# Optimization experiments

Hardware: AMD Instinct MI355X
Metric: run time of the kernel (lower is better)

## Reference

```python
import jax, jax.numpy as jnp
import numpy as np
from jax import lax

SCALE_R = 1.0
LOCAL_MAX_THR = 0.1
BORDER = 5
MAX_NUM_CENTERS = 2048  # 16 * 128
DILATIONS = (1, 4, 16)
NEG_INF = -1e9


def _conv2d(x, w, d):
    # x: [B,1,H,W], w: [1,1,3,3], dilation d, SAME padding
    return lax.conv_general_dilated(
        x, w, window_strides=(1, 1), padding='SAME', rhs_dilation=(d, d),
        dimension_numbers=('NCHW', 'OIHW', 'NCHW'))


def _avg3(x):
    s = lax.reduce_window(x, 0.0, lax.add, (1, 1, 3, 3), (1, 1, 1, 1), 'SAME')
    return s * (1.0 / 9.0)


def _maxpool3(x):
    return lax.reduce_window(x, -jnp.inf, lax.max, (1, 1, 3, 3), (1, 1, 1, 1), 'SAME')


def setup_inputs() -> dict:
    key = jax.random.key(0)
    k1, k2, k3 = jax.random.split(key, 3)
    inp = jax.random.normal(k1, (8, 3, 1024, 1024), dtype=jnp.float32)
    w_c = jax.random.normal(k2, (3, 1, 1, 3, 3), dtype=jnp.float32) * 0.1
    w_s = jax.random.normal(k3, (3, 1, 1, 3, 3), dtype=jnp.float32) * 0.1
    return {'input': inp, 'w_c': w_c, 'w_s': w_s}


def reference(input, w_c, w_s):
    B, _, H, W = input.shape
    S = input[:, 0:1]          # sin direction field
    C = input[:, 1:2]          # cos direction field
    # R = inverse_log_r(scale_r * R_raw) = exp(scale_r * r) - 1
    R = jnp.exp(SCALE_R * input[:, 2:3]) - 1.0
    output = jnp.concatenate([S, C, R], axis=1)  # input with R channel replaced

    # multiscale localization: learned 3x3 convs at several dilations over C and S
    resp = jnp.zeros_like(S)
    for i, d in enumerate(DILATIONS):
        resp = resp + _conv2d(C, w_c[i], d) + _conv2d(S, w_s[i], d)
    conv_resp = jax.nn.relu(resp)  # [B,1,H,W] center heatmap

    # local-max selection: smooth, compare against 3x3 max, threshold, exclude border
    smooth = _avg3(conv_resp)
    is_peak = (smooth >= _maxpool3(smooth)) & (smooth > LOCAL_MAX_THR)
    border = jnp.zeros((H, W), dtype=bool).at[BORDER:H - BORDER, BORDER:W - BORDER].set(True)
    is_peak = is_peak & border[None, None]

    # per-batch top-K centers by response score (vectorized NMS/top-k)
    flat = conv_resp.reshape(B, H * W)
    scores = jnp.where(is_peak.reshape(B, H * W), flat, NEG_INF)
    vals, idx = lax.top_k(scores, MAX_NUM_CENTERS)          # [B, K]
    valid = (vals > LOCAL_MAX_THR).astype(flat.dtype)
    x = (idx % W).astype(flat.dtype) * valid
    y = (idx // W).astype(flat.dtype) * valid
    v = vals * valid
    # packed centers: [valid_flag, x, y, score, score] -> [B, K, 5]
    center_pred = jnp.stack([valid, x, y, v, v], axis=-1)
    return output, center_pred, conv_resp
```

## Files before the change

kernel.cpp:

```cpp
#include <hip/hip_runtime.h>
#include <cstdint>

typedef unsigned int u32;
typedef unsigned long long u64;

#define BATCH 8
#define H 1024
#define W 1024
#define HW (H*W)
#define NPIX (BATCH*HW)
#define KTOP 2048
#define NBIN 8192
#define KEYCAP 8192
#define CAPP 131072
#define CAPC 65536
#define TARGET 2080

#define D9 1e-3f
#define DV 1e-4f

#define TOX 64
#define TOY 32
#define CCX 72
#define CCY 36
#define SCSTR 76
#define SIROWS 68
#define SICOLS 104
#define SISTR 104
#define NJT 3
#define CAPB 768

#define MP(b) ((b)*16)
#define MC(b) (128 + (b)*16)
#define MK(b) (256 + (b)*16)
#define MT(b) (384 + (b)*16)

#define OFF_MISC 0
#define OFF_PASS 4096
#define OFF_CHK  (OFF_PASS + (size_t)BATCH*CAPP*8)
#define OFF_KEY  (OFF_CHK  + (size_t)BATCH*CAPC*8)

#define LD4(p) (*reinterpret_cast<const float4*>(p))
#define ST4(p,v) (*reinterpret_cast<float4*>(p) = (v))

__device__ __forceinline__ double conv_resp_f64(
    const float* __restrict__ in, const float* __restrict__ wc,
    const float* __restrict__ wsw, int b, int y, int x)
{
  const float* base = in + (size_t)b * 3 * HW;
  const float* Sp = base;
  const float* Cp = base + HW;
  double resp = 0.0;
  const int dil[3] = {1, 4, 16};
  #pragma unroll
  for (int di = 0; di < 3; ++di) {
    int d = dil[di];
    double ac = 0.0, as = 0.0;
    #pragma unroll
    for (int ky = 0; ky < 3; ++ky) {
      int yy = y + (ky - 1) * d;
      bool yok = ((unsigned)yy < (unsigned)H);
      #pragma unroll
      for (int kx = 0; kx < 3; ++kx) {
        int xx = x + (kx - 1) * d;
        bool ok = yok && ((unsigned)xx < (unsigned)W);
        double a  = ok ? (double)Cp[yy * W + xx] : 0.0;
        double s2 = ok ? (double)Sp[yy * W + xx] : 0.0;
        ac = fma(a,  (double)wc[di * 9 + ky * 3 + kx], ac);
        as = fma(s2, (double)wsw[di * 9 + ky * 3 + kx], as);
      }
    }
    resp += ac;
    resp += as;
  }
  return resp > 0.0 ? resp : 0.0;
}

__device__ __forceinline__ u64 make_key(double val, int p) {
  u64 dbits = __double_as_longlong(val);
  return (dbits & ~0xFFFFFull) | (u64)((~(u32)p) & 0xFFFFFu);
}

__device__ __forceinline__ void stage_ch(
    float* sIn, const float* __restrict__ src, int tx0, int ty0, int tid)
{
  const int NG = (SIROWS * SICOLS) / 4;
  for (int g = tid; g < NG; g += 256) {
    int r = g / (SICOLS / 4);
    int c4 = (g - r * (SICOLS / 4)) * 4;
    int gy = ty0 - 18 + r;
    int gx0 = tx0 - 20 + c4;
    float4 v = make_float4(0.f, 0.f, 0.f, 0.f);
    if ((unsigned)gy < (unsigned)H) {
      if (gx0 >= 0 && gx0 + 3 < W) {
        v = LD4(src + gy * W + gx0);
      } else {
        float t[4];
        #pragma unroll
        for (int i = 0; i < 4; ++i) {
          int gx = gx0 + i;
          t[i] = ((unsigned)gx < (unsigned)W) ? src[gy * W + gx] : 0.f;
        }
        v = make_float4(t[0], t[1], t[2], t[3]);
      }
    }
    *reinterpret_cast<float4*>(&sIn[r * SISTR + c4]) = v;
  }
}

__device__ __forceinline__ void accum_taps4(
    const float* sIn, const float* __restrict__ wp, float part[NJT][4], int tid)
{
  #pragma unroll
  for (int k = 0; k < NJT; ++k) {
    int j = k * 256 + tid;
    if (j < (CCX / 4) * CCY) {
      int cr = j / (CCX / 4);
      int cc0 = (j - cr * (CCX / 4)) * 4;
      const float* base = sIn + (cr + 16) * SISTR + cc0 + 16;

      float4 a1L = LD4(base - SISTR - 4),      a1M = LD4(base - SISTR),      a1R = LD4(base - SISTR + 4);
      float4 b1L = LD4(base + SISTR - 4),      b1M = LD4(base + SISTR),      b1R = LD4(base + SISTR + 4);
      float4 a4L = LD4(base - 4 * SISTR - 4),  a4M = LD4(base - 4 * SISTR),  a4R = LD4(base - 4 * SISTR + 4);
      float4 b4L = LD4(base + 4 * SISTR - 4),  b4M = LD4(base + 4 * SISTR),  b4R = LD4(base + 4 * SISTR + 4);
      float4 gAa = LD4(base - 16 * SISTR - 16), gAm = LD4(base - 16 * SISTR), gAb = LD4(base - 16 * SISTR + 16);
      float4 gBa = LD4(base + 16 * SISTR - 16), gBm = LD4(base + 16 * SISTR), gBb = LD4(base + 16 * SISTR + 16);
      float4 zA = LD4(base - 16), zL = LD4(base - 4), zM = LD4(base), zR = LD4(base + 4), zB = LD4(base + 16);

      float wm1[12] = {a1L.x,a1L.y,a1L.z,a1L.w, a1M.x,a1M.y,a1M.z,a1M.w, a1R.x,a1R.y,a1R.z,a1R.w};
      float wp1[12] = {b1L.x,b1L.y,b1L.z,b1L.w, b1M.x,b1M.y,b1M.z,b1M.w, b1R.x,b1R.y,b1R.z,b1R.w};
      float wm4[12] = {a4L.x,a4L.y,a4L.z,a4L.w, a4M.x,a4M.y,a4M.z,a4M.w, a4R.x,a4R.y,a4R.z,a4R.w};
      float wp4[12] = {b4L.x,b4L.y,b4L.z,b4L.w, b4M.x,b4M.y,b4M.z,b4M.w, b4R.x,b4R.y,b4R.z,b4R.w};
      float wz [12] = {zL.x,zL.y,zL.z,zL.w, zM.x,zM.y,zM.z,zM.w, zR.x,zR.y,zR.z,zR.w};
      float vAa[4] = {gAa.x,gAa.y,gAa.z,gAa.w};
      float vAm[4] = {gAm.x,gAm.y,gAm.z,gAm.w};
      float vAb[4] = {gAb.x,gAb.y,gAb.z,gAb.w};
      float vBa[4] = {gBa.x,gBa.y,gBa.z,gBa.w};
      float vBm[4] = {gBm.x,gBm.y,gBm.z,gBm.w};
      float vBb[4] = {gBb.x,gBb.y,gBb.z,gBb.w};
      float vzA[4] = {zA.x,zA.y,zA.z,zA.w};
      float vzB[4] = {zB.x,zB.y,zB.z,zB.w};

      #pragma unroll
      for (int i = 0; i < 4; ++i) {
        float ac = 0.f;
        ac = fmaf(wm1[i + 3], wp[0], ac);
        ac = fmaf(wm1[i + 4], wp[1], ac);
        ac = fmaf(wm1[i + 5], wp[2], ac);
        ac = fmaf(wz [i + 3], wp[3], ac);
        ac = fmaf(wz [i + 4], wp[4], ac);
        ac = fmaf(wz [i + 5], wp[5], ac);
        ac = fmaf(wp1[i + 3], wp[6], ac);
        ac = fmaf(wp1[i + 4], wp[7], ac);
        ac = fmaf(wp1[i + 5], wp[8], ac);
        float a = ac;
        ac = 0.f;
        ac = fmaf(wm4[i + 0], wp[9],  ac);
        ac = fmaf(wm4[i + 4], wp[10], ac);
        ac = fmaf(wm4[i + 8], wp[11], ac);
        ac = fmaf(wz [i + 0], wp[12], ac);
        ac = fmaf(wz [i + 4], wp[13], ac);
        ac = fmaf(wz [i + 8], wp[14], ac);
        ac = fmaf(wp4[i + 0], wp[15], ac);
        ac = fmaf(wp4[i + 4], wp[16], ac);
        ac = fmaf(wp4[i + 8], wp[17], ac);
        a += ac;
        ac = 0.f;
        ac = fmaf(vAa[i], wp[18], ac);
        ac = fmaf(vAm[i], wp[19], ac);
        ac = fmaf(vAb[i], wp[20], ac);
        ac = fmaf(vzA[i], wp[21], ac);
        ac = fmaf(wz[i + 4], wp[22], ac);
        ac = fmaf(vzB[i], wp[23], ac);
        ac = fmaf(vBa[i], wp[24], ac);
        ac = fmaf(vBm[i], wp[25], ac);
        ac = fmaf(vBb[i], wp[26], ac);
        a += ac;
        part[k][i] += a;
      }
    }
  }
}

__global__ __launch_bounds__(256, 4) void conv_screen_kernel(
    const float* __restrict__ in, const float* __restrict__ wc,
    const float* __restrict__ wsw, float* __restrict__ out0,
    float* __restrict__ convr, u64* __restrict__ passlist,
    u64* __restrict__ checklist, u32* __restrict__ misc)
{
  __shared__ __align__(16) float uni[SIROWS * SISTR];

  float* sIn = uni;
  float (*sconv)[SCSTR] = (float (*)[SCSTR])uni;
  u64* pbuf = (u64*)(uni + 2752);
  u64* cbuf = (u64*)(uni + 2752 + 2 * CAPB);
  u32* lcnt = (u32*)(uni + 2752 + 4 * CAPB);

  int b = blockIdx.z;
  int tx0 = blockIdx.x * TOX;
  int ty0 = blockIdx.y * TOY;
  int tid = threadIdx.x;
  const float* Sp = in + (size_t)b * 3 * HW;
  const float* Cp = Sp + HW;
  const float* Rp = Sp + 2 * HW;
  float* ob = out0 + (size_t)b * 3 * HW;
  float* cb = convr + (size_t)b * HW;

  #pragma unroll
  for (int r = 0; r < (TOX * TOY) / 4 / 256; ++r) {
    int idx = r * 256 + tid;
    int ly = idx / (TOX / 4);
    int lx4 = (idx - ly * (TOX / 4)) * 4;
    int p0 = (ty0 + ly) * W + tx0 + lx4;
    float4 S4 = LD4(Sp + p0);
    float4 C4 = LD4(Cp + p0);
    float4 R4 = LD4(Rp + p0);
    ST4(ob + p0, S4);
    ST4(ob + HW + p0, C4);
    float4 E4 = make_float4(expf(R4.x) - 1.f, expf(R4.y) - 1.f,
                            expf(R4.z) - 1.f, expf(R4.w) - 1.f);
    ST4(ob + 2 * HW + p0, E4);
  }

  float part[NJT][4];
  #pragma unroll
  for (int k = 0; k < NJT; ++k)
    #pragma unroll
    for (int i = 0; i < 4; ++i) part[k][i] = 0.f;

  stage_ch(sIn, Cp, tx0, ty0, tid);
  __syncthreads();
  accum_taps4(sIn, wc, part, tid);
  __syncthreads();
  stage_ch(sIn, Sp, tx0, ty0, tid);
  __syncthreads();
  accum_taps4(sIn, wsw, part, tid);
  __syncthreads();

  if (tid < 4) lcnt[tid] = 0;
  #pragma unroll
  for (int k = 0; k < NJT; ++k) {
    int j = k * 256 + tid;
    if (j < (CCX / 4) * CCY) {
      int cr = j / (CCX / 4);
      int cc0 = (j - cr * (CCX / 4)) * 4;
      float4 rv = make_float4(fmaxf(part[k][0], 0.f), fmaxf(part[k][1], 0.f),
                              fmaxf(part[k][2], 0.f), fmaxf(part[k][3], 0.f));
      *reinterpret_cast<float4*>(&sconv[cr][cc0]) = rv;
      if (cr >= 2 && cr <= CCY - 3 && cc0 >= 4 && cc0 <= 64) {
        int gy = ty0 - 2 + cr, gx0 = tx0 - 4 + cc0;
        ST4(cb + gy * W + gx0, rv);
      }
    }
  }
  __syncthreads();

  for (int r = 0; r < (TOX * TOY) / 256; ++r) {
    int idx = r * 256 + tid;
    int ly = idx >> 6;
    int lx = idx & 63;
    int x = tx0 + lx, y = ty0 + ly;
    bool act = (y >= 5 && y <= H - 6 && x >= 5 && x <= W - 6);

    bool cand = false, pass = false;
    float val = 0.f;
    if (act) {
      float vs0[5], vs1[5], vs2[5];
      #pragma unroll
      for (int j = 0; j < 5; ++j) {
        int c = lx + 2 + j;
        float a0 = sconv[ly + 0][c];
        float a1 = sconv[ly + 1][c];
        float a2 = sconv[ly + 2][c];
        float a3 = sconv[ly + 3][c];
        float a4 = sconv[ly + 4][c];
        vs0[j] = a0 + a1 + a2;
        vs1[j] = a1 + a2 + a3;
        vs2[j] = a2 + a3 + a4;
      }
      float hs0[3], hs1[3], hs2[3];
      #pragma unroll
      for (int j = 0; j < 3; ++j) {
        hs0[j] = vs0[j] + vs0[j + 1] + vs0[j + 2];
        hs1[j] = vs1[j] + vs1[j + 1] + vs1[j + 2];
        hs2[j] = vs2[j] + vs2[j + 1] + vs2[j + 2];
      }
      float sc9 = hs1[1];
      val = sconv[ly + 2][lx + 4];
      float m9 = fmaxf(fmaxf(fmaxf(hs0[0], hs0[1]), fmaxf(hs0[2], hs1[0])),
                       fmaxf(fmaxf(hs1[2], hs2[0]), fmaxf(hs2[1], hs2[2])));
      cand = !((sc9 < 0.9f - D9) || (sc9 < m9 - D9) || (val < 0.1f - DV));
      pass = cand && (sc9 > 0.9f + D9) && (sc9 >= m9 + D9) && (val > 0.1f + DV);
    }

    u64 entry = ((u64)__float_as_uint(val) << 32) | (u32)(y * W + x);
    if (pass) {
      u32 pos = atomicAdd(&lcnt[0], 1u);
      if (pos < CAPB) pbuf[pos] = entry;
      else {
        u32 g = atomicAdd(&misc[MP(b)], 1u);
        if (g < CAPP) passlist[(size_t)b * CAPP + g] = entry;
      }
    } else if (cand) {
      u32 pos = atomicAdd(&lcnt[1], 1u);
      if (pos < CAPB) cbuf[pos] = entry;
      else {
        u32 g = atomicAdd(&misc[MC(b)], 1u);
        if (g < CAPC) checklist[(size_t)b * CAPC + g] = entry;
      }
    }
  }
  __syncthreads();

  u32 np = min(lcnt[0], (u32)CAPB);
  u32 nc = min(lcnt[1], (u32)CAPB);
  if (tid == 0) lcnt[2] = np ? atomicAdd(&misc[MP(b)], np) : 0u;
  if (tid == 1) lcnt[3] = nc ? atomicAdd(&misc[MC(b)], nc) : 0u;
  __syncthreads();
  u32 pbase = lcnt[2], cbase = lcnt[3];

  for (u32 i = tid; i < np; i += 256) {
    u32 g = pbase + i;
    if (g < CAPP) passlist[(size_t)b * CAPP + g] = pbuf[i];
  }
  for (u32 i = tid; i < nc; i += 256) {
    u32 g = cbase + i;
    if (g < CAPC) checklist[(size_t)b * CAPC + g] = cbuf[i];
  }
}

__global__ __launch_bounds__(1024) void cutscan_kernel(
    const u64* __restrict__ passlist, u32* __restrict__ misc)
{
  __shared__ u32 sfx[NBIN + NBIN / 32];
  #define SX(i) sfx[(i) + ((i) >> 5)]
  int b = blockIdx.x;
  int tid = threadIdx.x;

  #pragma unroll
  for (int k = 0; k < 8; ++k) SX(tid * 8 + k) = 0u;
  __syncthreads();

  int np = (int)min(misc[MP(b)], (u32)CAPP);
  const u64* L = passlist + (size_t)b * CAPP;
  for (int i = tid; i < np; i += 1024) {
    u32 vb = (u32)(L[i] >> 32);
    u32 bin = vb >> 19;
    atomicAdd(&sfx[bin + (bin >> 5)], 1u);
  }
  __syncthreads();

  for (int off = 1; off < NBIN; off <<= 1) {
    u32 t[8];
    #pragma unroll
    for (int k = 0; k < 8; ++k) {
      int i = tid * 8 + k;
      t[k] = (i + off < NBIN) ? SX(i + off) : 0u;
    }
    __syncthreads();
    #pragma unroll
    for (int k = 0; k < 8; ++k) SX(tid * 8 + k) += t[k];
    __syncthreads();
  }

  if (SX(0) < TARGET) return;

  #pragma unroll
  for (int k = 0; k < 8; ++k) {
    int i = tid * 8 + k;
    u32 s = SX(i);
    u32 nxt = (i + 1 < NBIN) ? SX(i + 1) : 0u;
    if (s >= TARGET && nxt < TARGET) {
      u32 cutbin = (i > 0) ? (u32)(i - 1) : 0u;
      misc[MT(b)] = cutbin << 19;
    }
  }
  #undef SX
}

__global__ __launch_bounds__(1024) void exact_kernel(
    const float* __restrict__ in, const float* __restrict__ wc,
    const float* __restrict__ wsw, const u64* __restrict__ passlist,
    const u64* __restrict__ checklist, u32* __restrict__ misc,
    u64* __restrict__ keybuf)
{
  int b = blockIdx.y;
  int sub = blockIdx.x;
  int tid = threadIdx.x;
  u32 cutb = misc[MT(b)];
  int lane = tid & 63;

  int np = (int)min(misc[MP(b)], (u32)CAPP);
  for (int i = sub * 1024 + tid; i < np; i += 16 * 1024) {
    u64 e = passlist[(size_t)b * CAPP + i];
    bool keep = ((u32)(e >> 32)) >= cutb;
    u64 k64 = 0;
    if (keep) {
      int p = (int)(e & 0xFFFFFu);
      k64 = make_key(conv_resp_f64(in, wc, wsw, b, p >> 10, p & (W - 1)), p);
    }
    u64 km = __ballot(keep);
    if (keep) {
      int leader = __ffsll((unsigned long long)km) - 1;
      u32 base = 0;
      if (lane == leader) base = atomicAdd(&misc[MK(b)], (u32)__popcll(km));
      base = __shfl(base, leader);
      u32 rk = (u32)__popcll(km & ((1ull << lane) - 1ull));
      if (base + rk < KEYCAP) keybuf[(size_t)b * KEYCAP + base + rk] = k64;
    }
  }

  int nc = (int)min(misc[MC(b)], (u32)CAPC);
  int wid = sub * 16 + (tid >> 6);
  for (int i = wid; i < nc; i += 256) {
    u64 e = checklist[(size_t)b * CAPC + i];
    if (((u32)(e >> 32)) < cutb) continue;
    int p = (int)(e & 0xFFFFFu);
    int y = p >> 10, x = p & (W - 1);

    double v = 0.0;
    if (lane < 25)
      v = conv_resp_f64(in, wc, wsw, b, y + lane / 5 - 2, x + lane % 5 - 2);

    double c[25];
    #pragma unroll
    for (int k = 0; k < 25; ++k) c[k] = __shfl(v, k);

    double cs0[5], cs1[5], cs2[5];
    #pragma unroll
    for (int j = 0; j < 5; ++j) {
      cs0[j] = c[0 + j] + c[5 + j] + c[10 + j];
      cs1[j] = c[5 + j] + c[10 + j] + c[15 + j];
      cs2[j] = c[10 + j] + c[15 + j] + c[20 + j];
    }
    double val = c[12];

    double sc = (cs1[1] + cs1[2] + cs1[3]) * (1.0 / 9.0);
    if (!(sc > 0.1)) continue;
    bool pk = true;
    #pragma unroll
    for (int j = 0; j < 3; ++j) {
      pk = pk && (sc >= (cs0[j] + cs0[j + 1] + cs0[j + 2]) * (1.0 / 9.0));
      pk = pk && (sc >= (cs2[j] + cs2[j + 1] + cs2[j + 2]) * (1.0 / 9.0));
    }
    pk = pk && (sc >= (cs1[0] + cs1[1] + cs1[2]) * (1.0 / 9.0));
    pk = pk && (sc >= (cs1[2] + cs1[3] + cs1[4]) * (1.0 / 9.0));
    if (!pk) continue;
    if (!(val > 0.1)) continue;

    if (lane == 0) {
      u32 pos = atomicAdd(&misc[MK(b)], 1u);
      if (pos < KEYCAP) keybuf[(size_t)b * KEYCAP + pos] = make_key(val, p);
    }
  }
}

__global__ __launch_bounds__(1024) void chunk_sort_kernel(
    u64* __restrict__ keybuf, const u32* __restrict__ misc)
{
  __shared__ u64 ck[1024];
  int b = blockIdx.y;
  int c = blockIdx.x;
  int tid = threadIdx.x;
  int M = (int)min(misc[MK(b)], (u32)KEYCAP);
  u64* base = keybuf + (size_t)b * KEYCAP;
  int gi = c * 1024 + tid;
  ck[tid] = (gi < M) ? base[gi] : 0ULL;
  __syncthreads();

  for (int k = 2; k <= 1024; k <<= 1) {
    for (int j = k >> 1; j > 0; j >>= 1) {
      int l = tid ^ j;
      if (l > tid) {
        u64 a = ck[tid], bb = ck[l];
        bool up = ((tid & k) == 0);
        bool sw = up ? (a < bb) : (a > bb);
        if (sw) { ck[tid] = bb; ck[l] = a; }
      }
      __syncthreads();
    }
  }
  base[gi] = ck[tid];
}

__global__ __launch_bounds__(1024) void merge_rank_kernel(
    const u64* __restrict__ keybuf, const u32* __restrict__ misc,
    const float* __restrict__ convr, float* __restrict__ center)
{
  __shared__ u64 sk[KEYCAP];
  int b = blockIdx.x;
  int tid = threadIdx.x;
  const u64* kb = keybuf + (size_t)b * KEYCAP;
  for (int i = tid; i < KEYCAP; i += 1024) sk[i] = kb[i];

  float* cb = center + (size_t)b * KTOP * 5;
  for (int i = tid; i < KTOP * 5; i += 1024) cb[i] = 0.f;
  __syncthreads();

  #pragma unroll
  for (int e = 0; e < KEYCAP / 1024; ++e) {
    int i = e * 1024 + tid;
    u64 k = sk[i];
    if (k == 0ULL) continue;
    int myc = i >> 10;
    int rank = i & 1023;
    #pragma unroll
    for (int c = 0; c < 8; ++c) {
      if (c == myc) continue;
      const u64* arr = &sk[c << 10];
      int lo = 0, hi = 1024;
      while (lo < hi) {
        int mid = (lo + hi) >> 1;
        if (arr[mid] > k) lo = mid + 1; else hi = mid;
      }
      rank += lo;
    }
    if (rank < KTOP) {
      u32 p = (~(u32)k) & 0xFFFFFu;
      float v = convr[(size_t)b * HW + p];
      float* o = cb + (size_t)rank * 5;
      o[0] = 1.0f;
      o[1] = (float)(p & (W - 1));
      o[2] = (float)(p >> 10);
      o[3] = v;
      o[4] = v;
    }
  }
}

extern "C" void kernel_launch(void* const* d_in, const int* in_sizes, int n_in,
                              void* d_out, int out_size, void* d_ws, size_t ws_size,
                              hipStream_t stream) {
  const float* in  = (const float*)d_in[0];
  const float* wc  = (const float*)d_in[1];
  const float* wsw = (const float*)d_in[2];

  float* out0   = (float*)d_out;
  float* center = out0 + (size_t)BATCH * 3 * HW;
  float* convr  = center + (size_t)BATCH * KTOP * 5;

  char* w = (char*)d_ws;
  u32* misc      = (u32*)(w + OFF_MISC);
  u64* passlist  = (u64*)(w + OFF_PASS);
  u64* checklist = (u64*)(w + OFF_CHK);
  u64* keybuf    = (u64*)(w + OFF_KEY);

  hipMemsetAsync(w, 0, OFF_PASS, stream);

  conv_screen_kernel<<<dim3(W / TOX, H / TOY, BATCH), 256, 0, stream>>>(
      in, wc, wsw, out0, convr, passlist, checklist, misc);
  cutscan_kernel<<<BATCH, 1024, 0, stream>>>(passlist, misc);
  exact_kernel<<<dim3(16, BATCH), 1024, 0, stream>>>(
      in, wc, wsw, passlist, checklist, misc, keybuf);
  chunk_sort_kernel<<<dim3(KEYCAP / 1024, BATCH), 1024, 0, stream>>>(keybuf, misc);
  merge_rank_kernel<<<BATCH, 1024, 0, stream>>>(keybuf, misc, convr, center);
}
```

Measured before the change: 226.1 us.

## Fuse chunk sort and merge-rank via last-block atomic counter; pad shared stride

Merges the per-chunk bitonic sort and the merge-rank kernels into one launch. The last block to finish sorting for each batch, found through an atomic counter in the misc workspace, performs the cross-chunk rank merge. This removes one kernel launch and the gap between launches, but every chunk block now allocates the full 64KB shared buffer, which can limit occupancy. A separate change pads a shared-memory row stride from 104 to 108 to reduce bank conflicts in the conv stage.

```diff
diff --git a/kernel.cpp b/kernel.cpp
--- a/kernel.cpp
+++ b/kernel.cpp
@@ -26,7 +26,7 @@
 #define SCSTR 76
 #define SIROWS 68
 #define SICOLS 104
-#define SISTR 104
+#define SISTR 108
 #define NJT 3
 #define CAPB 768
 
@@ -34,6 +34,7 @@
 #define MC(b) (128 + (b)*16)
 #define MK(b) (256 + (b)*16)
 #define MT(b) (384 + (b)*16)
+#define MD(b) (512 + (b)*16)
 
 #define OFF_MISC 0
 #define OFF_PASS 4096
@@ -455,43 +456,48 @@
   }
 }
 
-__global__ __launch_bounds__(1024) void chunk_sort_kernel(
-    u64* __restrict__ keybuf, const u32* __restrict__ misc)
-{
-  __shared__ u64 ck[1024];
+__global__ __launch_bounds__(1024) void sort_merge_kernel(
+    u64* __restrict__ keybuf, u32* __restrict__ misc,
+    const float* __restrict__ convr, float* __restrict__ center)
+{
+  __shared__ u64 sk[KEYCAP];
+  __shared__ u32 lastflag;
   int b = blockIdx.y;
   int c = blockIdx.x;
   int tid = threadIdx.x;
   int M = (int)min(misc[MK(b)], (u32)KEYCAP);
   u64* base = keybuf + (size_t)b * KEYCAP;
   int gi = c * 1024 + tid;
-  ck[tid] = (gi < M) ? base[gi] : 0ULL;
+  sk[tid] = (gi < M) ? base[gi] : 0ULL;
   __syncthreads();
 
   for (int k = 2; k <= 1024; k <<= 1) {
     for (int j = k >> 1; j > 0; j >>= 1) {
       int l = tid ^ j;
       if (l > tid) {
-        u64 a = ck[tid], bb = ck[l];
+        u64 a = sk[tid], bb = sk[l];
         bool up = ((tid & k) == 0);
         bool sw = up ? (a < bb) : (a > bb);
-        if (sw) { ck[tid] = bb; ck[l] = a; }
+        if (sw) { sk[tid] = bb; sk[l] = a; }
       }
       __syncthreads();
     }
   }
-  base[gi] = ck[tid];
-}
-
-__global__ __launch_bounds__(1024) void merge_rank_kernel(
-    const u64* __restrict__ keybuf, const u32* __restrict__ misc,
-    const float* __restrict__ convr, float* __restrict__ center)
-{
-  __shared__ u64 sk[KEYCAP];
-  int b = blockIdx.x;
-  int tid = threadIdx.x;
-  const u64* kb = keybuf + (size_t)b * KEYCAP;
-  for (int i = tid; i < KEYCAP; i += 1024) sk[i] = kb[i];
+  base[gi] = sk[tid];
+  __syncthreads();
+
+  if (tid == 0) {
+    __threadfence();
+    u32 done = atomicAdd(&misc[MD(b)], 1u);
+    lastflag = (done == KEYCAP / 1024 - 1) ? 1u : 0u;
+  }
+  __syncthreads();
+  if (!lastflag) return;
+
+  if (tid == 0) __threadfence();
+  __syncthreads();
+
+  for (int i = tid; i < KEYCAP; i += 1024) sk[i] = base[i];
 
   float* cb = center + (size_t)b * KTOP * 5;
   for (int i = tid; i < KTOP * 5; i += 1024) cb[i] = 0.f;
@@ -505,9 +511,9 @@
     int myc = i >> 10;
     int rank = i & 1023;
     #pragma unroll
-    for (int c = 0; c < 8; ++c) {
-      if (c == myc) continue;
-      const u64* arr = &sk[c << 10];
+    for (int cc = 0; cc < 8; ++cc) {
+      if (cc == myc) continue;
+      const u64* arr = &sk[cc << 10];
       int lo = 0, hi = 1024;
       while (lo < hi) {
         int mid = (lo + hi) >> 1;
@@ -552,6 +558,6 @@
   cutscan_kernel<<<BATCH, 1024, 0, stream>>>(passlist, misc);
   exact_kernel<<<dim3(16, BATCH), 1024, 0, stream>>>(
       in, wc, wsw, passlist, checklist, misc, keybuf);
-  chunk_sort_kernel<<<dim3(KEYCAP / 1024, BATCH), 1024, 0, stream>>>(keybuf, misc);
-  merge_rank_kernel<<<BATCH, 1024, 0, stream>>>(keybuf, misc, convr, center);
-}
+  sort_merge_kernel<<<dim3(KEYCAP / 1024, BATCH), 1024, 0, stream>>>(
+      keybuf, misc, convr, center);
+}
```

After: 230.1 us. No clear change (+1.8%).
